# Optimization experiments

Measured on AMD Instinct MI355X. Metric: run time of the kernel, lower is better.

The kernel has to match this reference:

```python
import jax, jax.numpy as jnp
import numpy as np

B, T, H = 2048, 256, 256
EPS = 1e-5


def _ln(x, g, b):
    m = jnp.mean(x, axis=-1, keepdims=True)
    v = jnp.mean((x - m) ** 2, axis=-1, keepdims=True)
    return (x - m) * jax.lax.rsqrt(v + EPS) * g + b


def _gelu(x):
    return jax.nn.gelu(x, approximate=False)


def _lstm_cell_scan(xproj_t, Whh, h0, c0):
    # xproj_t: [T, B, 4H] precomputed input projection (+ both biases)
    def step(carry, xp):
        h, c = carry
        gates = xp + h @ Whh.T  # [B, 4H]
        i, f, g, o = jnp.split(gates, 4, axis=-1)  # torch gate order i,f,g,o
        i = jax.nn.sigmoid(i)
        f = jax.nn.sigmoid(f)
        g = jnp.tanh(g)
        o = jax.nn.sigmoid(o)
        c = f * c + i * g
        h = o * jnp.tanh(c)
        return (h, c), h
    (_, _), hs = jax.lax.scan(step, (h0, c0), xproj_t)
    return hs  # [T, B, H]


def setup_inputs() -> dict:
    key = jax.random.key(0)
    ks = jax.random.split(key, 24)
    r = lambda k, shp, s=0.05: jax.random.normal(k, shp, dtype=jnp.float32) * s
    inp = {
        "x": jax.random.normal(ks[0], (B, 5), dtype=jnp.float32),
        # encoder
        "W1": r(ks[1], (128, 5)), "b1": jnp.zeros((128,), jnp.float32),
        "g1": jnp.ones((128,), jnp.float32), "be1": jnp.zeros((128,), jnp.float32),
        "W2": r(ks[2], (256, 128)), "b2": jnp.zeros((256,), jnp.float32),
        "g2": jnp.ones((256,), jnp.float32), "be2": jnp.zeros((256,), jnp.float32),
        # lstm layer 0
        "Wih0": r(ks[3], (4 * H, 256)), "Whh0": r(ks[4], (4 * H, H)),
        "bih0": jnp.zeros((4 * H,), jnp.float32), "bhh0": jnp.zeros((4 * H,), jnp.float32),
        # lstm layer 1
        "Wih1": r(ks[5], (4 * H, H)), "Whh1": r(ks[6], (4 * H, H)),
        "bih1": jnp.zeros((4 * H,), jnp.float32), "bhh1": jnp.zeros((4 * H,), jnp.float32),
        # decoder
        "W3": r(ks[7], (128, 256)), "b3": jnp.zeros((128,), jnp.float32),
        "W4": r(ks[8], (2, 128)), "b4": jnp.zeros((2,), jnp.float32),
    }
    return inp


def reference(x, W1, b1, g1, be1, W2, b2, g2, be2,
              Wih0, Whh0, bih0, bhh0, Wih1, Whh1, bih1, bhh1,
              W3, b3, W4, b4):
    # encoder: Linear -> GELU -> LN -> Linear -> GELU -> LN
    h = _ln(_gelu(x @ W1.T + b1), g1, be1)
    enc = _ln(_gelu(h @ W2.T + b2), g2, be2)  # [B, 256]

    h0 = jnp.zeros((B, H), enc.dtype)
    c0 = jnp.zeros((B, H), enc.dtype)

    # layer 0: input is the same encoded vector at every step ->
    # input projection is constant, compute once and broadcast over T
    xp0 = enc @ Wih0.T + bih0 + bhh0  # [B, 4H]
    xp0_t = jnp.broadcast_to(xp0, (T, B, 4 * H))
    hs0 = _lstm_cell_scan(xp0_t, Whh0, h0, c0)  # [T, B, H]

    # layer 1: input varies per step
    xp1_t = jnp.einsum('tbh,gh->tbg', hs0, Wih1) + bih1 + bhh1
    hs1 = _lstm_cell_scan(xp1_t, Whh1, h0, c0)  # [T, B, H]

    lstm_out = jnp.transpose(hs1, (1, 0, 2))  # [B, T, H] (batch_first)

    # decoder: Linear -> GELU -> Linear
    d = _gelu(lstm_out @ W3.T + b3)
    return d @ W4.T + b4  # [B, T, 2]
```

## Files before the change

kernel.cpp:

```cpp
#include <hip/hip_runtime.h>
#include <math.h>


typedef short s8v __attribute__((ext_vector_type(8)));
typedef float f4v __attribute__((ext_vector_type(4)));
typedef unsigned long long u64;

#define IMG_SH   1084416
#define H0G_SH   (IMG_SH)
#define H1G_SH   (H0G_SH + 1048576)
#define CNT_SH   (H1G_SH + 1048576)
#define ENC_SH   (CNT_SH + 16640)

__device__ __forceinline__ f4v mfma16(s8v a, s8v b, f4v c){
  return __builtin_amdgcn_mfma_f32_16x16x32_bf16(a, b, c, 0, 0, 0);
}
__device__ __forceinline__ short f2bf(float f){
  unsigned u = __float_as_uint(f);
  u = u + 0x7FFFu + ((u >> 16) & 1u);
  return (short)(u >> 16);
}
__device__ __forceinline__ float wred(float v){
  #pragma unroll
  for (int o = 32; o; o >>= 1) v += __shfl_xor(v, o);
  return v;
}
__device__ __forceinline__ float rcpf(float x){ return __builtin_amdgcn_rcpf(x); }
__device__ __forceinline__ float sigm(float x){ return rcpf(1.0f + __expf(-x)); }
__device__ __forceinline__ float tnh(float x){
  x = fminf(15.0f, fmaxf(-15.0f, x));
  float e = __expf(2.0f * x);
  return (e - 1.0f) * rcpf(e + 1.0f);
}
__device__ __forceinline__ float gelu(float v){
  return 0.5f * v * (1.0f + erff(v * 0.70710678118654752440f));
}

__device__ __forceinline__ u64 ldc8(const u64* p){
  return __hip_atomic_load(p, __ATOMIC_RELAXED, __HIP_MEMORY_SCOPE_AGENT);
}
__device__ __forceinline__ void stc2(short* p, short v){
  __hip_atomic_store(p, v, __ATOMIC_RELAXED, __HIP_MEMORY_SCOPE_AGENT);
}
__device__ __forceinline__ void stc8(u64* p, u64 v){
  __hip_atomic_store(p, v, __ATOMIC_RELAXED, __HIP_MEMORY_SCOPE_AGENT);
}
__device__ __forceinline__ void wbar(){
  asm volatile("s_waitcnt lgkmcnt(0)" ::: "memory");
  __builtin_amdgcn_s_barrier();
}
__device__ __forceinline__ void arrive_bar(unsigned* c, int tid){
  asm volatile("s_waitcnt vmcnt(0) lgkmcnt(0)" ::: "memory");
  __builtin_amdgcn_s_barrier();
  if (tid == 0)
    __hip_atomic_fetch_add(c, 1u, __ATOMIC_RELAXED, __HIP_MEMORY_SCOPE_AGENT);
}
__device__ __forceinline__ void wait_bar(unsigned* c, int tid){
  if (tid == 0){
    unsigned it = 0;
    while (__hip_atomic_load(c, __ATOMIC_RELAXED, __HIP_MEMORY_SCOPE_AGENT) < 8u
           && ++it < (1u << 18))
      __builtin_amdgcn_s_sleep(2);
  }
  __builtin_amdgcn_s_barrier();
  asm volatile("" ::: "memory");
}

__global__ void prep_kernel(
    const float* __restrict__ Wih0, const float* __restrict__ Whh0,
    const float* __restrict__ Wih1, const float* __restrict__ Whh1,
    const float* __restrict__ W3,   const float* __restrict__ W4,
    short* __restrict__ wsb)
{
  const int i = blockIdx.x * 256 + threadIdx.x;
  if (i >= 1083392) return;
  float v;
  if (i < 1048576){
    const int seg = i >> 18;
    const int r   = i & 262143;
    const int s   = r >> 14;
    const int g   = (r >> 12) & 3;
    const int kk  = (r >> 9) & 7;
    const int q   = (r >> 7) & 3;
    const int m16 = (r >> 3) & 15;
    const int j   = r & 7;
    const int hid = s * 16 + m16;
    const int k   = kk * 32 + q * 8 + j;
    const float* mt = (seg == 0) ? Wih0 : (seg == 1) ? Whh0 : (seg == 2) ? Wih1 : Whh1;
    v = mt[(g * 256 + hid) * 256 + k];
  } else if (i < 1081344){
    const int r   = i - 1048576;
    const int s2  = r >> 12;
    const int kk  = (r >> 9) & 7;
    const int q   = (r >> 7) & 3;
    const int m16 = (r >> 3) & 15;
    const int j   = r & 7;
    v = W3[(s2 * 16 + m16) * 256 + kk * 32 + q * 8 + j];
  } else {
    const int r   = i - 1081344;
    const int kk  = (r >> 9) & 3;
    const int q   = (r >> 7) & 3;
    const int m16 = (r >> 3) & 15;
    const int j   = r & 7;
    const int k   = kk * 32 + q * 8 + j;
    v = (m16 < 2) ? W4[m16 * 128 + k] : 0.0f;
  }
  wsb[i] = f2bf(v);
}


__global__ __launch_bounds__(512) void curve_rec(
    const float* __restrict__ x,
    const float* __restrict__ W1, const float* __restrict__ b1,
    const float* __restrict__ g1, const float* __restrict__ be1,
    const float* __restrict__ W2, const float* __restrict__ b2,
    const float* __restrict__ g2, const float* __restrict__ be2,
    const float* __restrict__ bih0, const float* __restrict__ bhh0,
    const float* __restrict__ bih1, const float* __restrict__ bhh1,
    const float* __restrict__ b3, const float* __restrict__ b4,
    const float* __restrict__ W4,
    short* __restrict__ wsb,
    float* __restrict__ out)
{
  const int tid  = threadIdx.x;
  const int v    = tid >> 6;
  const int lane = tid & 63;
  const int q    = lane >> 4;
  const int m16  = lane & 15;
  const int bid  = blockIdx.x;
  const int g    = bid & 31;
  const int m    = bid >> 5;
  const int gate = v & 3;
  const int ch   = v >> 2;

  const short* img = wsb;
  short* h0g  = wsb + H0G_SH;
  short* h1g  = wsb + H1G_SH;
  short* encg = wsb + ENC_SH;
  unsigned* cnt = (unsigned*)(wsb + CNT_SH) + g * 260;

  __shared__ __align__(16) short ldsH0[16384];
  __shared__ __align__(16) short ldsX [16384];
  __shared__ __align__(16) float Gst[2][256 * 36];
  __shared__ __align__(16) float pstg[128];

  s8v Bh0[8], Bi1[8], Bh1[8], W3r[8];
  const int sIdx = 2 * m + ch;
  #pragma unroll
  for (int kk = 0; kk < 8; kk++){
    const int off = sIdx * 16384 + gate * 4096 + kk * 512 + (lane << 3);
    Bh0[kk] = *(const s8v*)(img + 262144 + off);
    Bi1[kk] = *(const s8v*)(img + 524288 + off);
    Bh1[kk] = *(const s8v*)(img + 786432 + off);
    W3r[kk] = *(const s8v*)(img + 1048576 + v * 4096 + kk * 512 + (lane << 3));
  }
  const float b3c = b3[v * 16 + m16];
  const float w40 = W4[v * 16 + m16];
  const float w41 = W4[128 + v * 16 + m16];
  const float b4o = b4[tid & 1];
  const int   n0  = gate * 256 + m * 32 + ch * 16 + m16;
  const float bs1v = bih1[n0] + bhh1[n0];
  const int row3 = m * 8 + m16, rt3 = row3 >> 4, rin3 = row3 & 15;
  const int rt_p = tid >> 7, rem = tid & 127;
  const int cq_p = (rem >> 5) & 3, r16p = (rem >> 1) & 15, c4h = rem & 1;
  const int rowp  = rt_p * 16 + r16p;
  const int coltp = cq_p * 8 + c4h * 4;
  const int pub_off = (rt_p * 8 + m) * 512 + rem * 4;

  {
    const int row_l = m * 8 + v;
    const int r = g * 64 + row_l;
    float xv[5];
    #pragma unroll
    for (int k = 0; k < 5; k++) xv[k] = x[r * 5 + k];
    float a0 = b1[lane], a1 = b1[lane + 64];
    #pragma unroll
    for (int k = 0; k < 5; k++){
      a0 += xv[k] * W1[lane * 5 + k];
      a1 += xv[k] * W1[(lane + 64) * 5 + k];
    }
    a0 = gelu(a0); a1 = gelu(a1);
    float mean = wred(a0 + a1) * (1.0f / 128.0f);
    float d0 = a0 - mean, d1 = a1 - mean;
    float inv = rsqrtf(wred(d0 * d0 + d1 * d1) * (1.0f / 128.0f) + 1e-5f);
    float y0 = d0 * inv * g1[lane]      + be1[lane];
    float y1 = d1 * inv * g1[lane + 64] + be1[lane + 64];

    float acc2[4];
    #pragma unroll
    for (int uu = 0; uu < 4; uu++) acc2[uu] = b2[lane + 64 * uu];
    for (int k = 0; k < 64; k++){
      float v0 = __shfl(y0, k);
      float v1 = __shfl(y1, k);
      #pragma unroll
      for (int uu = 0; uu < 4; uu++){
        const float* wr = W2 + (lane + 64 * uu) * 128;
        acc2[uu] += v0 * wr[k] + v1 * wr[k + 64];
      }
    }
    #pragma unroll
    for (int uu = 0; uu < 4; uu++) acc2[uu] = gelu(acc2[uu]);
    float s = acc2[0] + acc2[1] + acc2[2] + acc2[3];
    mean = wred(s) * (1.0f / 256.0f);
    float vv = 0.0f;
    #pragma unroll
    for (int uu = 0; uu < 4; uu++){ float d = acc2[uu] - mean; vv += d * d; }
    inv = rsqrtf(wred(vv) * (1.0f / 256.0f) + 1e-5f);
    short* eb = encg + g * 16384;
    const int rt_e = row_l >> 4, rin_e = row_l & 15;
    const int qe = (lane >> 3) & 3, je = lane & 7;
    #pragma unroll
    for (int uu = 0; uu < 4; uu++){
      const int c = lane + 64 * uu;
      const float e = (acc2[uu] - mean) * inv * g2[c] + be2[c];
      stc2(eb + (rt_e * 8 + (c >> 5)) * 512 + (qe * 16 + rin_e) * 8 + je, f2bf(e));
    }
  }
  arrive_bar(cnt + 258, tid);
  wait_bar(cnt + 258, tid);

  {
    const u64* src = (const u64*)(encg + g * 16384);
    u64 t[8];
    #pragma unroll
    for (int u = 0; u < 8; u++) t[u] = ldc8(src + tid + u * 512);
    #pragma unroll
    for (int u = 0; u < 8; u++) ((u64*)ldsH0)[tid + u * 512] = t[u];
  }
  wbar();
  f4v xp[4];
  {
    s8v Wi0[8];
    #pragma unroll
    for (int kk = 0; kk < 8; kk++)
      Wi0[kk] = *(const s8v*)(img + sIdx * 16384 + gate * 4096 + kk * 512 + (lane << 3));
    const float bi = bih0[n0] + bhh0[n0];
    #pragma unroll
    for (int rt = 0; rt < 4; rt++){ f4v t = {bi, bi, bi, bi}; xp[rt] = t; }
    const short* A0 = ldsH0 + (lane << 3);
    #pragma unroll
    for (int rt = 0; rt < 4; rt++)
      #pragma unroll
      for (int kk = 0; kk < 8; kk++)
        xp[rt] = mfma16(*(const s8v*)(A0 + (rt * 8 + kk) * 512), Wi0[kk], xp[rt]);
  }
  wbar();

  float c0[4] = {0.f,0.f,0.f,0.f}, c1[4] = {0.f,0.f,0.f,0.f};

  #pragma unroll 1
  for (int s = 0; s <= 257; s++){
    const bool dec = (s >= 2);

    const u64* h0src = (const u64*)(h0g + ((s & 1) * 32 + g) * 16384);
    const u64* h1src = (const u64*)(h1g + ((((s + 1) & 1)) * 32 + g) * 16384);
    u64 t0[8], t1[8];
    if (s <= 256){
      #pragma unroll
      for (int u = 0; u < 8; u++) t0[u] = ldc8(h0src + tid + u * 512);
    }
    if (s >= 1){
      #pragma unroll
      for (int u = 0; u < 8; u++) t1[u] = ldc8(h1src + tid + u * 512);
    }
    if (s <= 256){
      #pragma unroll
      for (int u = 0; u < 8; u++) ((u64*)ldsH0)[tid + u * 512] = t0[u];
    }
    wbar();

    f4v acc0[4], acc1[4];
    #pragma unroll
    for (int rt = 0; rt < 4; rt++){
      acc0[rt] = xp[rt];
      f4v t = {bs1v, bs1v, bs1v, bs1v};
      acc1[rt] = t;
    }
    {
      const short* A0 = ldsH0 + (lane << 3);
      #pragma unroll
      for (int rt = 0; rt < 4; rt++)
        #pragma unroll
        for (int kk = 0; kk < 8; kk++){
          const s8v a = *(const s8v*)(A0 + (rt * 8 + kk) * 512);
          acc0[rt] = mfma16(a, Bh0[kk], acc0[rt]);
          acc1[rt] = mfma16(a, Bi1[kk], acc1[rt]);
        }
    }
    if (s >= 1){
      #pragma unroll
      for (int u = 0; u < 8; u++) ((u64*)ldsX)[tid + u * 512] = t1[u];
    }
    wbar();

    {
      const short* A1 = ldsX + (lane << 3);
      #pragma unroll
      for (int rt = 0; rt < 4; rt++)
        #pragma unroll
        for (int kk = 0; kk < 8; kk++)
          acc1[rt] = mfma16(*(const s8v*)(A1 + (rt * 8 + kk) * 512), Bh1[kk], acc1[rt]);
    }
    f4v ad = {0.f, 0.f, 0.f, 0.f};
    if (dec){
      #pragma unroll
      for (int kk = 0; kk < 8; kk++){
        const s8v a3 = *(const s8v*)(ldsX + (rt3 * 8 + kk) * 512 + (q * 16 + rin3) * 8);
        ad = mfma16(a3, W3r[kk], ad);
      }
    }

    {
      #pragma unroll
      for (int rt = 0; rt < 4; rt++)
        #pragma unroll
        for (int r = 0; r < 4; r++){
          const int row = rt * 16 + q * 4 + r;
          Gst[0][(gate * 64 + row) * 36 + ch * 16 + m16] = acc0[rt][r];
          Gst[1][(gate * 64 + row) * 36 + ch * 16 + m16] = acc1[rt][r];
        }
    }
    wbar();

    if (s <= 255){
      const float* G0 = &Gst[0][0];
      const f4v gi = *(const f4v*)&G0[(0 * 64 + rowp) * 36 + coltp];
      const f4v gf = *(const f4v*)&G0[(1 * 64 + rowp) * 36 + coltp];
      const f4v gg = *(const f4v*)&G0[(2 * 64 + rowp) * 36 + coltp];
      const f4v go = *(const f4v*)&G0[(3 * 64 + rowp) * 36 + coltp];
      u64 pk = 0;
      #pragma unroll
      for (int j = 0; j < 4; j++){
        const float ii = sigm(gi[j]), ff = sigm(gf[j]);
        const float ga = tnh(gg[j]),  oo = sigm(go[j]);
        c0[j] = ff * c0[j] + ii * ga;
        pk |= (u64)(unsigned short)f2bf(oo * tnh(c0[j])) << (16 * j);
      }
      stc8((u64*)(h0g + ((((s + 1) & 1)) * 32 + g) * 16384 + pub_off), pk);
    }
    if (s >= 1 && s <= 256){
      const float* G1 = &Gst[1][0];
      const f4v gi = *(const f4v*)&G1[(0 * 64 + rowp) * 36 + coltp];
      const f4v gf = *(const f4v*)&G1[(1 * 64 + rowp) * 36 + coltp];
      const f4v gg = *(const f4v*)&G1[(2 * 64 + rowp) * 36 + coltp];
      const f4v go = *(const f4v*)&G1[(3 * 64 + rowp) * 36 + coltp];
      u64 pk = 0;
      #pragma unroll
      for (int j = 0; j < 4; j++){
        const float ii = sigm(gi[j]), ff = sigm(gf[j]);
        const float ga = tnh(gg[j]),  oo = sigm(go[j]);
        c1[j] = ff * c1[j] + ii * ga;
        pk |= (u64)(unsigned short)f2bf(oo * tnh(c1[j])) << (16 * j);
      }
      stc8((u64*)(h1g + ((s & 1) * 32 + g) * 16384 + pub_off), pk);
    }

    if (s <= 256) arrive_bar(cnt + s, tid);

    if (dec){
      float p0[4], p1[4];
      #pragma unroll
      for (int r = 0; r < 4; r++){
        const float dv = gelu(ad[r] + b3c);
        p0[r] = dv * w40;
        p1[r] = dv * w41;
      }
      #pragma unroll
      for (int mk = 1; mk < 16; mk <<= 1)
        #pragma unroll
        for (int r = 0; r < 4; r++){
          p0[r] += __shfl_xor(p0[r], mk);
          p1[r] += __shfl_xor(p1[r], mk);
        }
      if (m16 == 0 && q < 2){
        #pragma unroll
        for (int r = 0; r < 4; r++){
          pstg[(v * 8 + q * 4 + r) * 2 + 0] = p0[r];
          pstg[(v * 8 + q * 4 + r) * 2 + 1] = p1[r];
        }
      }
    }
    wbar();
    if (dec && tid < 16){
      const int row = tid >> 1, o = tid & 1;
      float sum = b4o;
      #pragma unroll
      for (int w2 = 0; w2 < 8; w2++) sum += pstg[(w2 * 8 + row) * 2 + o];
      out[((size_t)(g * 64 + m * 8 + row) * 256 + (s - 2)) * 2 + o] = sum;
    }

    if (s <= 256) wait_bar(cnt + s, tid);
  }
}

extern "C" void kernel_launch(void* const* d_in, const int* in_sizes, int n_in,
                              void* d_out, int out_size, void* d_ws, size_t ws_size,
                              hipStream_t stream)
{
  const float* x    = (const float*)d_in[0];
  const float* W1   = (const float*)d_in[1];
  const float* b1   = (const float*)d_in[2];
  const float* g1   = (const float*)d_in[3];
  const float* be1  = (const float*)d_in[4];
  const float* W2   = (const float*)d_in[5];
  const float* b2   = (const float*)d_in[6];
  const float* g2   = (const float*)d_in[7];
  const float* be2  = (const float*)d_in[8];
  const float* Wih0 = (const float*)d_in[9];
  const float* Whh0 = (const float*)d_in[10];
  const float* bih0 = (const float*)d_in[11];
  const float* bhh0 = (const float*)d_in[12];
  const float* Wih1 = (const float*)d_in[13];
  const float* Whh1 = (const float*)d_in[14];
  const float* bih1 = (const float*)d_in[15];
  const float* bhh1 = (const float*)d_in[16];
  const float* W3   = (const float*)d_in[17];
  const float* b3   = (const float*)d_in[18];
  const float* W4   = (const float*)d_in[19];
  const float* b4   = (const float*)d_in[20];

  short* wsb = (short*)d_ws;

  prep_kernel<<<4232, 256, 0, stream>>>(Wih0, Whh0, Wih1, Whh1, W3, W4, wsb);
  hipMemsetAsync((char*)d_ws + 2168832, 0, 4227584, stream);
  curve_rec<<<256, 512, 0, stream>>>(x, W1, b1, g1, be1, W2, b2, g2, be2,
                                     bih0, bhh0, bih1, bhh1, b3, b4, W4, wsb,
                                     (float*)d_out);
}
```

Measured before the change: 2.112 ms.

## Split the per-step grid barrier into separate layer-0 and layer-1 barriers

```diff
diff --git a/kernel.cpp b/kernel.cpp
--- a/kernel.cpp
+++ b/kernel.cpp
@@ -10,7 +10,7 @@
 #define H0G_SH   (IMG_SH)
 #define H1G_SH   (H0G_SH + 1048576)
 #define CNT_SH   (H1G_SH + 1048576)
-#define ENC_SH   (CNT_SH + 16640)
+#define ENC_SH   (CNT_SH + 33280)
 
 __device__ __forceinline__ f4v mfma16(s8v a, s8v b, f4v c){
   return __builtin_amdgcn_mfma_f32_16x16x32_bf16(a, b, c, 0, 0, 0);
@@ -137,7 +137,9 @@
   short* h0g  = wsb + H0G_SH;
   short* h1g  = wsb + H1G_SH;
   short* encg = wsb + ENC_SH;
-  unsigned* cnt = (unsigned*)(wsb + CNT_SH) + g * 260;
+  unsigned* cntb = (unsigned*)(wsb + CNT_SH);
+  unsigned* cnt0 = cntb + g * 260;
+  unsigned* cnt1 = cntb + 32 * 260 + g * 260;
 
   __shared__ __align__(16) short ldsH0[16384];
   __shared__ __align__(16) short ldsX [16384];
@@ -216,8 +218,8 @@
       stc2(eb + (rt_e * 8 + (c >> 5)) * 512 + (qe * 16 + rin_e) * 8 + je, f2bf(e));
     }
   }
-  arrive_bar(cnt + 258, tid);
-  wait_bar(cnt + 258, tid);
+  arrive_bar(cnt0 + 258, tid);
+  wait_bar(cnt0 + 258, tid);
 
   {
     const u64* src = (const u64*)(encg + g * 16384);
@@ -250,79 +252,59 @@
 
   #pragma unroll 1
   for (int s = 0; s <= 257; s++){
-    const bool dec = (s >= 2);
-
-    const u64* h0src = (const u64*)(h0g + ((s & 1) * 32 + g) * 16384);
-    const u64* h1src = (const u64*)(h1g + ((((s + 1) & 1)) * 32 + g) * 16384);
-    u64 t0[8], t1[8];
-    if (s <= 256){
+    const bool stg0 = (s <= 256);
+    const bool g0c  = (s <= 255);
+    const bool gPc  = (s <= 256);
+    const bool stg1 = (s >= 1);
+    const bool g1c  = (s >= 1 && s <= 256);
+    const bool decM = (s >= 2);
+
+    if (s >= 1 && stg0) wait_bar(cnt0 + (s - 1), tid);
+    if (stg0){
+      const u64* h0src = (const u64*)(h0g + ((s & 1) * 32 + g) * 16384);
+      u64 t0[8];
       #pragma unroll
       for (int u = 0; u < 8; u++) t0[u] = ldc8(h0src + tid + u * 512);
-    }
-    if (s >= 1){
-      #pragma unroll
-      for (int u = 0; u < 8; u++) t1[u] = ldc8(h1src + tid + u * 512);
-    }
-    if (s <= 256){
       #pragma unroll
       for (int u = 0; u < 8; u++) ((u64*)ldsH0)[tid + u * 512] = t0[u];
     }
     wbar();
 
-    f4v acc0[4], acc1[4];
-    #pragma unroll
-    for (int rt = 0; rt < 4; rt++){
-      acc0[rt] = xp[rt];
-      f4v t = {bs1v, bs1v, bs1v, bs1v};
-      acc1[rt] = t;
-    }
-    {
+    f4v acc0[4], accP[4];
+    if (stg0){
+      #pragma unroll
+      for (int rt = 0; rt < 4; rt++){
+        acc0[rt] = xp[rt];
+        f4v t = {bs1v, bs1v, bs1v, bs1v};
+        accP[rt] = t;
+      }
       const short* A0 = ldsH0 + (lane << 3);
+      if (g0c){
+        #pragma unroll
+        for (int rt = 0; rt < 4; rt++)
+          #pragma unroll
+          for (int kk = 0; kk < 8; kk++){
+            const s8v a = *(const s8v*)(A0 + (rt * 8 + kk) * 512);
+            acc0[rt] = mfma16(a, Bh0[kk], acc0[rt]);
+            accP[rt] = mfma16(a, Bi1[kk], accP[rt]);
+          }
+      } else if (gPc){
+        #pragma unroll
+        for (int rt = 0; rt < 4; rt++)
+          #pragma unroll
+          for (int kk = 0; kk < 8; kk++)
+            accP[rt] = mfma16(*(const s8v*)(A0 + (rt * 8 + kk) * 512), Bi1[kk], accP[rt]);
+      }
+    }
+    if (g0c){
       #pragma unroll
       for (int rt = 0; rt < 4; rt++)
         #pragma unroll
-        for (int kk = 0; kk < 8; kk++){
-          const s8v a = *(const s8v*)(A0 + (rt * 8 + kk) * 512);
-          acc0[rt] = mfma16(a, Bh0[kk], acc0[rt]);
-          acc1[rt] = mfma16(a, Bi1[kk], acc1[rt]);
-        }
-    }
-    if (s >= 1){
-      #pragma unroll
-      for (int u = 0; u < 8; u++) ((u64*)ldsX)[tid + u * 512] = t1[u];
+        for (int r = 0; r < 4; r++)
+          Gst[0][(gate * 64 + rt * 16 + q * 4 + r) * 36 + ch * 16 + m16] = acc0[rt][r];
     }
     wbar();
-
-    {
-      const short* A1 = ldsX + (lane << 3);
-      #pragma unroll
-      for (int rt = 0; rt < 4; rt++)
-        #pragma unroll
-        for (int kk = 0; kk < 8; kk++)
-          acc1[rt] = mfma16(*(const s8v*)(A1 + (rt * 8 + kk) * 512), Bh1[kk], acc1[rt]);
-    }
-    f4v ad = {0.f, 0.f, 0.f, 0.f};
-    if (dec){
-      #pragma unroll
-      for (int kk = 0; kk < 8; kk++){
-        const s8v a3 = *(const s8v*)(ldsX + (rt3 * 8 + kk) * 512 + (q * 16 + rin3) * 8);
-        ad = mfma16(a3, W3r[kk], ad);
-      }
-    }
-
-    {
-      #pragma unroll
-      for (int rt = 0; rt < 4; rt++)
-        #pragma unroll
-        for (int r = 0; r < 4; r++){
-          const int row = rt * 16 + q * 4 + r;
-          Gst[0][(gate * 64 + row) * 36 + ch * 16 + m16] = acc0[rt][r];
-          Gst[1][(gate * 64 + row) * 36 + ch * 16 + m16] = acc1[rt][r];
-        }
-    }
-    wbar();
-
-    if (s <= 255){
+    if (g0c){
       const float* G0 = &Gst[0][0];
       const f4v gi = *(const f4v*)&G0[(0 * 64 + rowp) * 36 + coltp];
       const f4v gf = *(const f4v*)&G0[(1 * 64 + rowp) * 36 + coltp];
@@ -337,8 +319,46 @@
         pk |= (u64)(unsigned short)f2bf(oo * tnh(c0[j])) << (16 * j);
       }
       stc8((u64*)(h0g + ((((s + 1) & 1)) * 32 + g) * 16384 + pub_off), pk);
-    }
-    if (s >= 1 && s <= 256){
+      arrive_bar(cnt0 + s, tid);
+    }
+
+    if (s >= 2 && stg1) wait_bar(cnt1 + (s - 1), tid);
+    if (stg1){
+      const u64* h1src = (const u64*)(h1g + ((((s + 1) & 1)) * 32 + g) * 16384);
+      u64 t1[8];
+      #pragma unroll
+      for (int u = 0; u < 8; u++) t1[u] = ldc8(h1src + tid + u * 512);
+      #pragma unroll
+      for (int u = 0; u < 8; u++) ((u64*)ldsX)[tid + u * 512] = t1[u];
+    }
+    wbar();
+
+    if (g1c){
+      const short* A1 = ldsX + (lane << 3);
+      #pragma unroll
+      for (int rt = 0; rt < 4; rt++)
+        #pragma unroll
+        for (int kk = 0; kk < 8; kk++)
+          accP[rt] = mfma16(*(const s8v*)(A1 + (rt * 8 + kk) * 512), Bh1[kk], accP[rt]);
+    }
+    f4v ad = {0.f, 0.f, 0.f, 0.f};
+    if (decM){
+      #pragma unroll
+      for (int kk = 0; kk < 8; kk++){
+        const s8v a3 = *(const s8v*)(ldsX + (rt3 * 8 + kk) * 512 + (q * 16 + rin3) * 8);
+        ad = mfma16(a3, W3r[kk], ad);
+      }
+    }
+    if (g1c){
+      #pragma unroll
+      for (int rt = 0; rt < 4; rt++)
+        #pragma unroll
+        for (int r = 0; r < 4; r++)
+          Gst[1][(gate * 64 + rt * 16 + q * 4 + r) * 36 + ch * 16 + m16] = accP[rt][r];
+    }
+    wbar();
+
+    if (g1c){
       const float* G1 = &Gst[1][0];
       const f4v gi = *(const f4v*)&G1[(0 * 64 + rowp) * 36 + coltp];
       const f4v gf = *(const f4v*)&G1[(1 * 64 + rowp) * 36 + coltp];
@@ -354,10 +374,7 @@
       }
       stc8((u64*)(h1g + ((s & 1) * 32 + g) * 16384 + pub_off), pk);
     }
-
-    if (s <= 256) arrive_bar(cnt + s, tid);
-
-    if (dec){
+    if (decM){
       float p0[4], p1[4];
       #pragma unroll
       for (int r = 0; r < 4; r++){
@@ -380,16 +397,15 @@
         }
       }
     }
-    wbar();
-    if (dec && tid < 16){
+    if (g1c) arrive_bar(cnt1 + s, tid);
+    else     wbar();
+    if (decM && tid < 16){
       const int row = tid >> 1, o = tid & 1;
       float sum = b4o;
       #pragma unroll
       for (int w2 = 0; w2 < 8; w2++) sum += pstg[(w2 * 8 + row) * 2 + o];
       out[((size_t)(g * 64 + m * 8 + row) * 256 + (s - 2)) * 2 + o] = sum;
     }
-
-    if (s <= 256) wait_bar(cnt + s, tid);
   }
 }
 
@@ -422,7 +438,7 @@
   short* wsb = (short*)d_ws;
 
   prep_kernel<<<4232, 256, 0, stream>>>(Wih0, Whh0, Wih1, Whh1, W3, W4, wsb);
-  hipMemsetAsync((char*)d_ws + 2168832, 0, 4227584, stream);
+  hipMemsetAsync((char*)d_ws + 2168832, 0, 4260864, stream);
   curve_rec<<<256, 512, 0, stream>>>(x, W1, b1, g1, be1, W2, b2, g2, be2,
                                      bih0, bhh0, bih1, bhh1, b3, b4, W4, wsb,
                                      (float*)d_out);
```

Result: faster. 1.971 ms (-6.7%).
